# Kernel optimization log

Hardware: AMD Instinct MI355X
Metric: run time of the kernel (lower is better)

The kernel has to match this reference:

```python
import jax, jax.numpy as jnp
import numpy as np

N, D_IN, D_OUT = 128, 512, 512
B = 256

def setup_inputs() -> dict:
    key = jax.random.key(0)
    kx, kw, kb = jax.random.split(key, 3)
    x = jax.random.normal(kx, (B, N, D_IN), dtype=jnp.float32)
    # nn.Linear default init: uniform(-1/sqrt(d_in), 1/sqrt(d_in)) for weight and bias
    bound = 1.0 / np.sqrt(D_IN)
    weight = jax.random.uniform(kw, (N, D_IN, D_OUT), dtype=jnp.float32, minval=-bound, maxval=bound)
    bias = jax.random.uniform(kb, (N, D_OUT), dtype=jnp.float32, minval=-bound, maxval=bound)
    return {"x": x, "weight": weight, "bias": bias}

def reference(x, weight, bias):
    # per-position linear: out[b,n,o] = sum_i x[b,n,i] * W[n,i,o] + bias[n,o]
    out = jnp.einsum('bni,nio->bno', x, weight)
    return out + bias[None]
```

## Files before the change

### kernel.cpp

```cpp
#include <hip/hip_runtime.h>

typedef __attribute__((ext_vector_type(8))) __bf16 bf16x8;
typedef __attribute__((ext_vector_type(4))) float f32x4;

#define DI 512
#define DO 512
#define XROW (128 * DI)
#define OROW (128 * DO)
#define BK 32
#define BOFF 16384
#define BUFSZ 32768

#define VMCNT(n) asm volatile("s_waitcnt vmcnt(" #n ")" ::: "memory")
#define LGKM0()  asm volatile("s_waitcnt lgkmcnt(0)" ::: "memory")
#define SBAR()   __builtin_amdgcn_s_barrier()
#define SCHED0() __builtin_amdgcn_sched_barrier(0)

__global__ __launch_bounds__(512, 4)
void nlinear_mfma(const float* __restrict__ xp, const float* __restrict__ wp,
                  const float* __restrict__ bp, float* __restrict__ op) {
  int blk = blockIdx.x;
  int L = ((blk & 7) << 6) + (blk >> 3);
  int n = L >> 2, mt = (L >> 1) & 1, ot = L & 1;
  int mBase = mt << 7, oBase = ot << 8;

  __shared__ char lds[2 * BUFSZ];

  int tid = threadIdx.x, lane = tid & 63, wid = tid >> 6;
  int wm = (wid >> 2) << 6, wn = (wid & 3) << 6;
  int l16 = lane & 15, l4 = lane >> 4;

  unsigned aOff[2];
  #pragma unroll
  for (int i = 0; i < 2; ++i) {
    int r0 = (wid << 4) + (i << 3);
    int row = r0 + (lane >> 3);
    int g = (lane & 7) ^ ((row >> 1) & 7);
    aOff[i] = (unsigned)(((mBase + row) * XROW + n * DI) * 4 + g * 16);
  }
  auto gloadA = [&](int bufOff, int kt) {
    #pragma unroll
    for (int i = 0; i < 2; ++i) {
      int r0 = (wid << 4) + (i << 3);
      __builtin_amdgcn_global_load_lds(
          (const __attribute__((address_space(1))) void*)
              ((const char*)xp + aOff[i] + (unsigned)(kt * 128)),
          (__attribute__((address_space(3))) void*)(lds + bufOff + r0 * 128),
          16, 0, 0);
    }
  };

  int bo = tid & 255, kh = tid >> 8;
  const float* bSrc = wp + ((size_t)n * DI + (kh << 4)) * DO + oBase + bo;
  int bWr0 = BOFF + bo * 64 + ((((kh << 1))     ^ ((bo >> 1) & 3)) << 4);
  int bWr1 = BOFF + bo * 64 + ((((kh << 1) | 1) ^ ((bo >> 1) & 3)) << 4);

  float bR[16];
  auto loadB = [&](int kt) {
    #pragma unroll
    for (int r = 0; r < 16; ++r)
      bR[r] = bSrc[(size_t)(kt * BK + r) * DO];
  };
  auto writeB = [&](int bufOff) {
    bf16x8 v0, v1;
    #pragma unroll
    for (int r = 0; r < 8; ++r) { v0[r] = (__bf16)bR[r]; v1[r] = (__bf16)bR[8 + r]; }
    *(bf16x8*)(lds + bufOff + bWr0) = v0;
    *(bf16x8*)(lds + bufOff + bWr1) = v1;
  };

  f32x4 acc[4][4];
  #pragma unroll
  for (int i = 0; i < 4; ++i)
    #pragma unroll
    for (int j = 0; j < 4; ++j)
      acc[i][j] = f32x4{0.f, 0.f, 0.f, 0.f};

  auto compute = [&](int bufOff) {
    bf16x8 af[4];
    #pragma unroll
    for (int i = 0; i < 4; ++i) {
      int row = wm + i * 16 + l16;
      int v7 = (row >> 1) & 7;
      const char* rb = lds + bufOff + row * 128;
      f32x4 lo = *(const f32x4*)(rb + ((((l4 << 1))     ^ v7) << 4));
      f32x4 hi = *(const f32x4*)(rb + ((((l4 << 1) | 1) ^ v7) << 4));
      af[i][0] = (__bf16)lo.x; af[i][1] = (__bf16)lo.y;
      af[i][2] = (__bf16)lo.z; af[i][3] = (__bf16)lo.w;
      af[i][4] = (__bf16)hi.x; af[i][5] = (__bf16)hi.y;
      af[i][6] = (__bf16)hi.z; af[i][7] = (__bf16)hi.w;
    }
    #pragma unroll
    for (int j = 0; j < 4; ++j) {
      int row = wn + j * 16 + l16;
      int slot = l4 ^ ((row >> 1) & 3);
      bf16x8 bfr = *(const bf16x8*)(lds + bufOff + BOFF + row * 64 + slot * 16);
      #pragma unroll
      for (int i = 0; i < 4; ++i)
        acc[i][j] = __builtin_amdgcn_mfma_f32_16x16x32_bf16(af[i], bfr, acc[i][j], 0, 0, 0);
    }
  };

  float bi[4];
  #pragma unroll
  for (int j = 0; j < 4; ++j)
    bi[j] = bp[n * DO + oBase + wn + j * 16 + l16];

  gloadA(0, 0);
  loadB(0);
  writeB(0);
  loadB(1);
  SCHED0(); LGKM0(); SBAR(); SCHED0();

  for (int kt = 0; kt < 14; ++kt) {
    int curOff = (kt & 1) * BUFSZ, nxtOff = curOff ^ BUFSZ;
    writeB(nxtOff);
    gloadA(nxtOff, kt + 1);
    loadB(kt + 2);
    compute(curOff);
    SCHED0();
    VMCNT(16);
    LGKM0(); SBAR(); SCHED0();
  }
  writeB(BUFSZ);
  gloadA(BUFSZ, 15);
  compute(0);
  SCHED0();
  VMCNT(0);
  LGKM0(); SBAR(); SCHED0();
  compute(BUFSZ);

  #pragma unroll
  for (int i = 0; i < 4; ++i) {
    #pragma unroll
    for (int j = 0; j < 4; ++j) {
      #pragma unroll
      for (int r = 0; r < 4; ++r) {
        int m = mBase + wm + i * 16 + l4 * 4 + r;
        int o = oBase + wn + j * 16 + l16;
        op[(size_t)m * OROW + n * DO + o] = acc[i][j][r] + bi[j];
      }
    }
  }
}

extern "C" void kernel_launch(void* const* d_in, const int* in_sizes, int n_in,
                              void* d_out, int out_size, void* d_ws, size_t ws_size,
                              hipStream_t stream) {
  const float* x = (const float*)d_in[0];
  const float* w = (const float*)d_in[1];
  const float* b = (const float*)d_in[2];
  float* o = (float*)d_out;
  hipLaunchKernelGGL(nlinear_mfma, dim3(512), dim3(512), 0, stream, x, w, b, o);
}
```

Measured before the change: 48.03 us.

## Vectorize weight loads to float2 and interleave global loads within MFMA compute

Each thread now loads two adjacent output columns of the weight tile with one float2 load, across 8 k-rows instead of 16 scalar loads. This halves the number of global load instructions for B and changes the LDS write pattern to two adjacent rows. The compute step is split into A-fragment loading plus per-column MFMA groups. Global A prefetch, the B LDS write and the next B load are issued between the first and second halves of the MFMAs to overlap memory with math. The vmcnt wait is lowered from 16 to 8 to match the smaller number of outstanding loads. The risks are a different LDS bank pattern for the B writes and extra register pressure from the hoisted A fragments.

Result: faster. 45.51 us (-5.3%).

```diff
diff --git a/kernel.cpp b/kernel.cpp
--- a/kernel.cpp
+++ b/kernel.cpp
@@ -2,6 +2,7 @@
 
 typedef __attribute__((ext_vector_type(8))) __bf16 bf16x8;
 typedef __attribute__((ext_vector_type(4))) float f32x4;
+typedef __attribute__((ext_vector_type(2))) float f32x2;
 
 #define DI 512
 #define DO 512
@@ -50,21 +51,21 @@
     }
   };
 
-  int bo = tid & 255, kh = tid >> 8;
-  const float* bSrc = wp + ((size_t)n * DI + (kh << 4)) * DO + oBase + bo;
-  int bWr0 = BOFF + bo * 64 + ((((kh << 1))     ^ ((bo >> 1) & 3)) << 4);
-  int bWr1 = BOFF + bo * 64 + ((((kh << 1) | 1) ^ ((bo >> 1) & 3)) << 4);
+  int bo2 = (tid & 127) << 1, kq = tid >> 7;
+  const float* bSrc = wp + ((size_t)n * DI + (kq << 3)) * DO + oBase + bo2;
+  int bWr0 = BOFF + (bo2)     * 64 + ((kq ^ ((bo2 >> 1) & 3)) << 4);
+  int bWr1 = BOFF + (bo2 + 1) * 64 + ((kq ^ ((bo2 >> 1) & 3)) << 4);
 
-  float bR[16];
+  f32x2 bRv[8];
   auto loadB = [&](int kt) {
     #pragma unroll
-    for (int r = 0; r < 16; ++r)
-      bR[r] = bSrc[(size_t)(kt * BK + r) * DO];
+    for (int j = 0; j < 8; ++j)
+      bRv[j] = *(const f32x2*)(bSrc + (size_t)(kt * BK + j) * DO);
   };
   auto writeB = [&](int bufOff) {
     bf16x8 v0, v1;
     #pragma unroll
-    for (int r = 0; r < 8; ++r) { v0[r] = (__bf16)bR[r]; v1[r] = (__bf16)bR[8 + r]; }
+    for (int j = 0; j < 8; ++j) { v0[j] = (__bf16)bRv[j].x; v1[j] = (__bf16)bRv[j].y; }
     *(bf16x8*)(lds + bufOff + bWr0) = v0;
     *(bf16x8*)(lds + bufOff + bWr1) = v1;
   };
@@ -76,8 +77,8 @@
     for (int j = 0; j < 4; ++j)
       acc[i][j] = f32x4{0.f, 0.f, 0.f, 0.f};
 
-  auto compute = [&](int bufOff) {
-    bf16x8 af[4];
+  bf16x8 af[4];
+  auto loadAfrags = [&](int bufOff) {
     #pragma unroll
     for (int i = 0; i < 4; ++i) {
       int row = wm + i * 16 + l16;
@@ -90,15 +91,14 @@
       af[i][4] = (__bf16)hi.x; af[i][5] = (__bf16)hi.y;
       af[i][6] = (__bf16)hi.z; af[i][7] = (__bf16)hi.w;
     }
+  };
+  auto computeJ = [&](int bufOff, int j) {
+    int row = wn + j * 16 + l16;
+    int slot = l4 ^ ((row >> 1) & 3);
+    bf16x8 bfr = *(const bf16x8*)(lds + bufOff + BOFF + row * 64 + slot * 16);
     #pragma unroll
-    for (int j = 0; j < 4; ++j) {
-      int row = wn + j * 16 + l16;
-      int slot = l4 ^ ((row >> 1) & 3);
-      bf16x8 bfr = *(const bf16x8*)(lds + bufOff + BOFF + row * 64 + slot * 16);
-      #pragma unroll
-      for (int i = 0; i < 4; ++i)
-        acc[i][j] = __builtin_amdgcn_mfma_f32_16x16x32_bf16(af[i], bfr, acc[i][j], 0, 0, 0);
-    }
+    for (int i = 0; i < 4; ++i)
+      acc[i][j] = __builtin_amdgcn_mfma_f32_16x16x32_bf16(af[i], bfr, acc[i][j], 0, 0, 0);
   };
 
   float bi[4];
@@ -114,21 +114,33 @@
 
   for (int kt = 0; kt < 14; ++kt) {
     int curOff = (kt & 1) * BUFSZ, nxtOff = curOff ^ BUFSZ;
+    loadAfrags(curOff);
+    computeJ(curOff, 0);
+    computeJ(curOff, 1);
+    gloadA(nxtOff, kt + 1);
     writeB(nxtOff);
-    gloadA(nxtOff, kt + 1);
     loadB(kt + 2);
-    compute(curOff);
     SCHED0();
-    VMCNT(16);
+    computeJ(curOff, 2);
+    computeJ(curOff, 3);
+    SCHED0();
+    VMCNT(8);
     LGKM0(); SBAR(); SCHED0();
   }
-  writeB(BUFSZ);
-  gloadA(BUFSZ, 15);
-  compute(0);
-  SCHED0();
-  VMCNT(0);
-  LGKM0(); SBAR(); SCHED0();
-  compute(BUFSZ);
+  {
+    loadAfrags(0);
+    computeJ(0, 0); computeJ(0, 1);
+    gloadA(BUFSZ, 15);
+    writeB(BUFSZ);
+    SCHED0();
+    computeJ(0, 2); computeJ(0, 3);
+    SCHED0();
+    VMCNT(0);
+    LGKM0(); SBAR(); SCHED0();
+  }
+  loadAfrags(BUFSZ);
+  computeJ(BUFSZ, 0); computeJ(BUFSZ, 1);
+  computeJ(BUFSZ, 2); computeJ(BUFSZ, 3);
 
   #pragma unroll
   for (int i = 0; i < 4; ++i) {
```
